# Kernel optimization log

Measured on AMD Instinct MI355X. Metric: run time of the kernel, lower is better.

The kernel has to match this reference:

```python
import jax, jax.numpy as jnp
import numpy as np

N_NODES = 50000
IN_DIM = 256
OUT_DIM = 128
NUM_HEADS = 2
N_EDGES = 800000


def setup_inputs() -> dict:
    key = jax.random.key(0)
    k1, k2, k3, k4, k5 = jax.random.split(key, 5)
    x = jax.random.normal(k1, (N_NODES, IN_DIM), dtype=jnp.float32)
    edge_index = jax.random.randint(k2, (2, N_EDGES), 0, N_NODES, dtype=jnp.int64)
    # Linear(in_dim, out_dim*num_heads): store weight as [in_dim, out_dim*num_heads]
    fan = IN_DIM + OUT_DIM * NUM_HEADS
    W_w = jax.random.uniform(k3, (IN_DIM, OUT_DIM * NUM_HEADS), dtype=jnp.float32,
                             minval=-np.sqrt(6.0 / fan), maxval=np.sqrt(6.0 / fan))
    W_b = jnp.zeros((OUT_DIM * NUM_HEADS,), dtype=jnp.float32)
    # attention vector a: [2*out_dim], xavier uniform over (1, 2*out_dim)
    fa = 1 + 2 * OUT_DIM
    a = jax.random.uniform(k4, (2 * OUT_DIM,), dtype=jnp.float32,
                           minval=-np.sqrt(6.0 / fa), maxval=np.sqrt(6.0 / fa))
    return {"x": x, "edge_index": edge_index, "W_w": W_w, "W_b": W_b, "a": a}


def _gat_forward(x, edge_index, W_w, W_b, a):
    N = x.shape[0]
    H, D = NUM_HEADS, OUT_DIM
    Wh = (x @ W_w + W_b).reshape(N, H, D)  # [N, H, D]
    src, dst = edge_index[0], edge_index[1]
    a_src, a_dst = a[:D], a[D:]
    # per-node partial scores, then gather -> avoids [E, 2D] concat
    s = jnp.einsum('nhd,d->nh', Wh, a_src)  # [N, H]
    t = jnp.einsum('nhd,d->nh', Wh, a_dst)  # [N, H]
    e = jax.nn.leaky_relu(s[src] + t[dst], negative_slope=0.2)  # [E, H]
    # segment softmax over edges grouped by src node
    m = jax.ops.segment_max(e, src, num_segments=N)  # [N, H], -inf for empty
    ex = jnp.exp(e - m[src])
    denom = jax.ops.segment_sum(ex, src, num_segments=N)  # [N, H]
    alpha = ex / denom[src]  # [E, H]
    # weighted aggregation of destination features into source nodes
    agg = jax.ops.segment_sum(alpha[:, :, None] * Wh[dst], src, num_segments=N)  # [N, H, D]
    deg = jax.ops.segment_sum(jnp.ones_like(src, dtype=Wh.dtype), src, num_segments=N)  # [N]
    h_prime = jnp.where(deg[:, None, None] > 0, agg, Wh)
    return h_prime.reshape(N, H * D)


def reference(x, edge_index, W_w, W_b, a):
    return _gat_forward(x, edge_index, W_w, W_b, a)
```

## Files before the change

### kernel.cpp

```cpp
#include <hip/hip_runtime.h>
#include <hip/hip_bf16.h>
#include <math.h>

#define N_NODES 50000
#define IN_DIM 256
#define OUT_DIM 128
#define NUM_HEADS 2
#define N_EDGES 800000
#define F (OUT_DIM*NUM_HEADS)
#define SCAN_B 1024
#define N_SB ((N_NODES + SCAN_B - 1) / SCAN_B)
#define LDSP 264
#define CAP 128
#define N_COPIES 8
#define NBLK ((N_NODES + 63) / 64)
#define GSZ (NBLK * 256)

typedef __bf16 bf16;
typedef __bf16 bf16x8 __attribute__((ext_vector_type(8)));
typedef float  f32x4  __attribute__((ext_vector_type(4)));
typedef unsigned short u16x8 __attribute__((ext_vector_type(8)));

__global__ void k_transpose(const float* __restrict__ W, bf16* __restrict__ Wt,
                            int* __restrict__ deg8) {
    int k = blockIdx.x;
    int n = threadIdx.x;
    Wt[(size_t)n*IN_DIM + k] = (bf16)W[(size_t)k*F + n];
    int id = blockIdx.x * F + threadIdx.x;
    for (int i = id; i < N_COPIES * N_NODES; i += IN_DIM * F)
        deg8[i] = 0;
}

__global__ __launch_bounds__(256) void k_gemm(const float* __restrict__ X,
                                              const bf16* __restrict__ Wt,
                                              const float* __restrict__ Wb,
                                              const float* __restrict__ Av,
                                              const int* __restrict__ src,
                                              int* __restrict__ deg8,
                                              unsigned char* __restrict__ rank,
                                              int* __restrict__ xcdtab,
                                              bf16* __restrict__ Wh,
                                              float* __restrict__ s_arr,
                                              float* __restrict__ t_arr) {
    __shared__ bf16 As[64 * LDSP];
    __shared__ float sS[2][64], sT[2][64];
    int t = threadIdx.x;
    int wave = t >> 6, lane = t & 63;
    int quad = lane >> 4, l16 = lane & 15;
    int row0 = blockIdx.x * 64;
    int col0 = wave * 64;
    int h = wave >> 1;

    {
        unsigned xcc;
        asm volatile("s_getreg_b32 %0, hwreg(HW_REG_XCC_ID, 0, 4)" : "=s"(xcc));
        xcc &= (N_COPIES - 1);
        if (t == 0) xcdtab[blockIdx.x] = (int)xcc;
        int* mydeg = deg8 + (size_t)xcc * N_NODES;
        int gid = blockIdx.x * 256 + t;
        for (int e = gid; e < N_EDGES; e += GSZ) {
            int s = src[e];
            int r = __hip_atomic_fetch_add(&mydeg[s], 1, __ATOMIC_RELAXED,
                                           __HIP_MEMORY_SCOPE_WORKGROUP);
            rank[e] = (unsigned char)r;
        }
    }

    {
        int rr = t >> 5;
        int cc = (t & 31) * 8;
        #pragma unroll
        for (int i = 0; i < 8; ++i) {
            int r = row0 + 8*i + rr;
            r = (r < N_NODES) ? r : (N_NODES - 1);
            const float* p = X + (size_t)r * IN_DIM + cc;
            f32x4 lo = *(const f32x4*)p;
            f32x4 hi = *(const f32x4*)(p + 4);
            bf16x8 pk;
            #pragma unroll
            for (int q = 0; q < 4; ++q) {
                pk[q]   = (bf16)lo[q];
                pk[q+4] = (bf16)hi[q];
            }
            *(bf16x8*)(As + (8*i + rr) * LDSP + cc) = pk;
        }
    }
    if (t < 128) { sS[t >> 6][t & 63] = 0.f; sT[t >> 6][t & 63] = 0.f; }
    __syncthreads();

    f32x4 acc[4][4] = {};
    #pragma unroll
    for (int ks = 0; ks < 8; ++ks) {
        int kb = ks * 32;
        bf16x8 bfrag[4];
        #pragma unroll
        for (int ni = 0; ni < 4; ++ni)
            bfrag[ni] = *(const bf16x8*)(Wt + (size_t)(col0 + ni*16 + l16)*IN_DIM
                                            + kb + quad*8);
        bf16x8 afrag[4];
        #pragma unroll
        for (int mi = 0; mi < 4; ++mi)
            afrag[mi] = *(const bf16x8*)(As + (mi*16 + l16)*LDSP + kb + quad*8);

        #pragma unroll
        for (int mi = 0; mi < 4; ++mi)
            #pragma unroll
            for (int ni = 0; ni < 4; ++ni)
                acc[mi][ni] = __builtin_amdgcn_mfma_f32_16x16x32_bf16(
                                  afrag[mi], bfrag[ni], acc[mi][ni], 0, 0, 0);
    }

    float bias_l[4], as_l[4], at_l[4];
    #pragma unroll
    for (int ni = 0; ni < 4; ++ni) {
        int c = col0 + ni*16 + l16;
        int d = c & (OUT_DIM - 1);
        bias_l[ni] = Wb[c];
        as_l[ni]   = Av[d];
        at_l[ni]   = Av[OUT_DIM + d];
    }

    #pragma unroll
    for (int mi = 0; mi < 4; ++mi) {
        #pragma unroll
        for (int reg = 0; reg < 4; ++reg) {
            int rl = mi*16 + quad*4 + reg;
            float ps = 0.f, pt = 0.f;
            #pragma unroll
            for (int ni = 0; ni < 4; ++ni) {
                float val = acc[mi][ni][reg] + bias_l[ni];
                ps += val * as_l[ni];
                pt += val * at_l[ni];
            }
            #pragma unroll
            for (int m = 8; m >= 1; m >>= 1) {
                ps += __shfl_xor(ps, m);
                pt += __shfl_xor(pt, m);
            }
            if ((lane & 15) == 0) {
                atomicAdd(&sS[h][rl], ps);
                atomicAdd(&sT[h][rl], pt);
            }
        }
    }

    __syncthreads();
    #pragma unroll
    for (int mi = 0; mi < 4; ++mi)
        #pragma unroll
        for (int ni = 0; ni < 4; ++ni) {
            int cc = col0 + ni*16 + l16;
            #pragma unroll
            for (int reg = 0; reg < 4; ++reg) {
                int rl = mi*16 + quad*4 + reg;
                As[rl*LDSP + cc] = (bf16)(acc[mi][ni][reg] + bias_l[ni]);
            }
        }
    __syncthreads();

    #pragma unroll
    for (int i = 0; i < 8; ++i) {
        int idx = i * 2048 + t * 8;
        int row = idx >> 8;
        int cc  = idx & 255;
        bf16x8 v = *(const bf16x8*)(As + row*LDSP + cc);
        int grow = row0 + row;
        if (grow < N_NODES)
            *(bf16x8*)(Wh + (size_t)grow*F + cc) = v;
    }

    if (t < 128) {
        int hh = t >> 6, rl = t & 63;
        int n = row0 + rl;
        if (n < N_NODES) {
            s_arr[n*2 + hh] = sS[hh][rl];
            t_arr[n*2 + hh] = sT[hh][rl];
        }
    }
}

__global__ __launch_bounds__(SCAN_B) void k_scan_local(const int* __restrict__ deg8,
                                                       int* __restrict__ excl,
                                                       int* __restrict__ bsum,
                                                       unsigned short* __restrict__ prefix8) {
    __shared__ int lds[SCAN_B];
    int t = threadIdx.x;
    int i = blockIdx.x * SCAN_B + t;
    int v = 0;
    if (i < N_NODES) {
        u16x8 pf;
        int run = 0;
        #pragma unroll
        for (int c = 0; c < N_COPIES; ++c) {
            pf[c] = (unsigned short)run;
            run += deg8[(size_t)c * N_NODES + i];
        }
        v = run;
        *(u16x8*)(prefix8 + (size_t)i * 8) = pf;
    }
    lds[t] = v;
    __syncthreads();
    for (int off = 1; off < SCAN_B; off <<= 1) {
        int u = (t >= off) ? lds[t - off] : 0;
        __syncthreads();
        lds[t] += u;
        __syncthreads();
    }
    if (i < N_NODES) excl[i] = lds[t] - v;
    if (t == SCAN_B - 1) bsum[blockIdx.x] = lds[t];
}

__global__ __launch_bounds__(256) void k_scan_final(const int* __restrict__ excl,
                                                    const int* __restrict__ bsum,
                                                    int* __restrict__ row_start) {
    __shared__ int sboff[64];
    int t = threadIdx.x;
    if (t < 64) {
        int orig = (t < N_SB) ? bsum[t] : 0;
        int v = orig;
        #pragma unroll
        for (int off = 1; off < 64; off <<= 1) {
            int u = __shfl_up(v, off);
            if (t >= off) v += u;
        }
        sboff[t] = v - orig;
        if (t == 63 && blockIdx.x == 0) row_start[N_NODES] = v;
    }
    __syncthreads();
    int i = blockIdx.x * 256 + t;
    if (i < N_NODES)
        row_start[i] = excl[i] + sboff[i >> 10];
}

__global__ __launch_bounds__(256) void k_scatter(const int* __restrict__ src,
                                                 const int* __restrict__ dst,
                                                 const unsigned char* __restrict__ rank,
                                                 const unsigned short* __restrict__ prefix8,
                                                 const int* __restrict__ row_start,
                                                 const int* __restrict__ xcdtab,
                                                 int* __restrict__ sorted_dst) {
    int e = blockIdx.x * 256 + threadIdx.x;
    if (e < N_EDGES) {
        int c = xcdtab[(e % GSZ) >> 8];
        int s = src[e];
        int pos = row_start[s] + (int)prefix8[(size_t)s * 8 + c] + (int)rank[e];
        sorted_dst[pos] = dst[e];
    }
}

__global__ __launch_bounds__(256) void k_agg(const bf16* __restrict__ Wh,
                                             const float* __restrict__ s_arr,
                                             const float* __restrict__ t_arr,
                                             const int* __restrict__ row_start,
                                             const int* __restrict__ sdst,
                                             float* __restrict__ out) {
    __shared__ float sp0[4][CAP];
    __shared__ float sp1[4][CAP];
    __shared__ int   sd[4][CAP];
    int wave = threadIdx.x >> 6, lane = threadIdx.x & 63;
    int n = blockIdx.x * 4 + wave;
    int sub = lane >> 5, cl = lane & 31;
    int c = cl * 8, h = cl >> 4;
    int beg = row_start[n], end = row_start[n + 1];
    if (beg == end) {
        if (sub == 0) {
            bf16x8 wh = *(const bf16x8*)(Wh + (size_t)n*F + c);
            f32x4 o0, o1;
            #pragma unroll
            for (int i = 0; i < 4; ++i) { o0[i] = (float)wh[i]; o1[i] = (float)wh[4+i]; }
            *(f32x4*)(out + (size_t)n*F + c)     = o0;
            *(f32x4*)(out + (size_t)n*F + c + 4) = o1;
        }
        return;
    }
    float2 sv = ((const float2*)s_arr)[n];
    float sum0 = 0.f, sum1 = 0.f;
    float a[8] = {0,0,0,0,0,0,0,0};
    float bacc[8] = {0,0,0,0,0,0,0,0};
    const float* sph = h ? sp1[wave] : sp0[wave];

    for (int c0 = beg; c0 < end; c0 += CAP) {
        int cnt = min(CAP, end - c0);
        for (int j = lane; j < cnt; j += 64) {
            int d = sdst[c0 + j];
            float2 tv = ((const float2*)t_arr)[d];
            float e0 = sv.x + tv.x; e0 = (e0 >= 0.f) ? e0 : 0.2f * e0;
            float e1 = sv.y + tv.y; e1 = (e1 >= 0.f) ? e1 : 0.2f * e1;
            float p0 = __expf(e0), p1 = __expf(e1);
            sp0[wave][j] = p0;
            sp1[wave][j] = p1;
            sd[wave][j]  = d;
            sum0 += p0;
            sum1 += p1;
        }
        int j = 0;
        for (; j + 8 <= cnt; j += 8) {
            int j0 = j + sub, j1 = j + 2 + sub, j2 = j + 4 + sub, j3 = j + 6 + sub;
            int d0 = sd[wave][j0], d1 = sd[wave][j1];
            int d2 = sd[wave][j2], d3 = sd[wave][j3];
            float p0 = sph[j0], p1 = sph[j1], p2 = sph[j2], p3 = sph[j3];
            bf16x8 w0 = *(const bf16x8*)(Wh + (size_t)d0*F + c);
            bf16x8 w1 = *(const bf16x8*)(Wh + (size_t)d1*F + c);
            bf16x8 w2 = *(const bf16x8*)(Wh + (size_t)d2*F + c);
            bf16x8 w3 = *(const bf16x8*)(Wh + (size_t)d3*F + c);
            #pragma unroll
            for (int i = 0; i < 8; ++i) {
                a[i]    += p0 * (float)w0[i];
                bacc[i] += p1 * (float)w1[i];
                a[i]    += p2 * (float)w2[i];
                bacc[i] += p3 * (float)w3[i];
            }
        }
        for (; j < cnt; j += 2) {
            int jj = j + sub;
            int jc = (jj < cnt) ? jj : 0;
            float p = (jj < cnt) ? sph[jc] : 0.f;
            int d = sd[wave][jc];
            bf16x8 w = *(const bf16x8*)(Wh + (size_t)d*F + c);
            #pragma unroll
            for (int i = 0; i < 8; ++i) a[i] += p * (float)w[i];
        }
    }
    #pragma unroll
    for (int m = 32; m >= 1; m >>= 1) {
        sum0 += __shfl_xor(sum0, m);
        sum1 += __shfl_xor(sum1, m);
    }
    float inv = 1.f / (h ? sum1 : sum0);
    #pragma unroll
    for (int i = 0; i < 8; ++i) {
        a[i] += bacc[i];
        a[i] += __shfl_xor(a[i], 32);
    }
    if (sub == 0) {
        f32x4 o0, o1;
        #pragma unroll
        for (int i = 0; i < 4; ++i) { o0[i] = a[i] * inv; o1[i] = a[4+i] * inv; }
        *(f32x4*)(out + (size_t)n*F + c)     = o0;
        *(f32x4*)(out + (size_t)n*F + c + 4) = o1;
    }
}

extern "C" void kernel_launch(void* const* d_in, const int* in_sizes, int n_in,
                              void* d_out, int out_size, void* d_ws, size_t ws_size,
                              hipStream_t stream) {
    const float* x  = (const float*)d_in[0];
    const int*   ei = (const int*)d_in[1];
    const float* Ww = (const float*)d_in[2];
    const float* Wb = (const float*)d_in[3];
    const float* a  = (const float*)d_in[4];
    float* out = (float*)d_out;
    const int* src = ei;
    const int* dst = ei + N_EDGES;

    char* ws = (char*)d_ws;
    bf16*  Wh        = (bf16*)ws;   ws += (size_t)N_NODES * F * 2;
    bf16*  Wt        = (bf16*)ws;   ws += (size_t)IN_DIM * F * 2;
    float* s_arr     = (float*)ws;  ws += (size_t)N_NODES * 2 * 4;
    float* t_arr     = (float*)ws;  ws += (size_t)N_NODES * 2 * 4;
    int*   excl      = (int*)ws;    ws += (size_t)N_NODES * 4;
    int*   bsum      = (int*)ws;    ws += 64 * 4;
    int*   row_start = (int*)ws;    ws += (size_t)(N_NODES + 1) * 4 + 12;
    unsigned short* prefix8 = (unsigned short*)ws; ws += (size_t)N_NODES * 8 * 2;
    unsigned char*  rank    = (unsigned char*)ws;  ws += (size_t)N_EDGES + 16;
    int*   xcdtab    = (int*)ws;    ws += (size_t)NBLK * 4 + 8;
    int*   sdst      = (int*)ws;    ws += (size_t)N_EDGES * 4;

    int* deg8 = sdst;

    k_transpose<<<IN_DIM, F, 0, stream>>>(Ww, Wt, deg8);
    k_gemm<<<NBLK, 256, 0, stream>>>(x, Wt, Wb, a, src, deg8, rank, xcdtab,
                                     Wh, s_arr, t_arr);
    k_scan_local<<<N_SB, SCAN_B, 0, stream>>>(deg8, excl, bsum, prefix8);
    k_scan_final<<<(N_NODES + 255) / 256, 256, 0, stream>>>(excl, bsum, row_start);
    k_scatter<<<(N_EDGES + 255) / 256, 256, 0, stream>>>(src, dst, rank, prefix8,
                                                         row_start, xcdtab, sdst);
    k_agg<<<N_NODES / 4, 256, 0, stream>>>(Wh, s_arr, t_arr, row_start, sdst, out);
}
```

Before: 244.9 us.

## Split edge histogram out of GEMM into a dedicated per-edge kernel

Moves the per-XCC source-degree atomic histogram and rank computation from the GEMM kernel's prologue into a separate kernel with one thread per edge. The scatter kernel now indexes the XCC table by block index directly and drops the modulo and bounds check. This is meant to remove the atomic work and grid-stride loop from the GEMM's critical path, at the cost of an extra kernel launch and losing the overlap between histogramming and GEMM loads.

```diff
diff --git a/kernel.cpp b/kernel.cpp
--- a/kernel.cpp
+++ b/kernel.cpp
@@ -13,8 +13,7 @@
 #define LDSP 264
 #define CAP 128
 #define N_COPIES 8
-#define NBLK ((N_NODES + 63) / 64)
-#define GSZ (NBLK * 256)
+#define NBLK_H (N_EDGES / 256)
 
 typedef __bf16 bf16;
 typedef __bf16 bf16x8 __attribute__((ext_vector_type(8)));
@@ -31,14 +30,25 @@
         deg8[i] = 0;
 }
 
+__global__ __launch_bounds__(256) void k_hist(const int* __restrict__ src,
+                                              int* __restrict__ deg8,
+                                              unsigned char* __restrict__ rank,
+                                              int* __restrict__ xcdtab) {
+    unsigned xcc;
+    asm volatile("s_getreg_b32 %0, hwreg(HW_REG_XCC_ID, 0, 4)" : "=s"(xcc));
+    xcc &= (N_COPIES - 1);
+    if (threadIdx.x == 0) xcdtab[blockIdx.x] = (int)xcc;
+    int e = blockIdx.x * 256 + threadIdx.x;
+    int s = src[e];
+    int r = __hip_atomic_fetch_add(&deg8[(size_t)xcc * N_NODES + s], 1,
+                                   __ATOMIC_RELAXED, __HIP_MEMORY_SCOPE_WORKGROUP);
+    rank[e] = (unsigned char)r;
+}
+
 __global__ __launch_bounds__(256) void k_gemm(const float* __restrict__ X,
                                               const bf16* __restrict__ Wt,
                                               const float* __restrict__ Wb,
                                               const float* __restrict__ Av,
-                                              const int* __restrict__ src,
-                                              int* __restrict__ deg8,
-                                              unsigned char* __restrict__ rank,
-                                              int* __restrict__ xcdtab,
                                               bf16* __restrict__ Wh,
                                               float* __restrict__ s_arr,
                                               float* __restrict__ t_arr) {
@@ -52,21 +62,6 @@
     int h = wave >> 1;
 
     {
-        unsigned xcc;
-        asm volatile("s_getreg_b32 %0, hwreg(HW_REG_XCC_ID, 0, 4)" : "=s"(xcc));
-        xcc &= (N_COPIES - 1);
-        if (t == 0) xcdtab[blockIdx.x] = (int)xcc;
-        int* mydeg = deg8 + (size_t)xcc * N_NODES;
-        int gid = blockIdx.x * 256 + t;
-        for (int e = gid; e < N_EDGES; e += GSZ) {
-            int s = src[e];
-            int r = __hip_atomic_fetch_add(&mydeg[s], 1, __ATOMIC_RELAXED,
-                                           __HIP_MEMORY_SCOPE_WORKGROUP);
-            rank[e] = (unsigned char)r;
-        }
-    }
-
-    {
         int rr = t >> 5;
         int cc = (t & 31) * 8;
         #pragma unroll
@@ -240,12 +235,10 @@
                                                  const int* __restrict__ xcdtab,
                                                  int* __restrict__ sorted_dst) {
     int e = blockIdx.x * 256 + threadIdx.x;
-    if (e < N_EDGES) {
-        int c = xcdtab[(e % GSZ) >> 8];
-        int s = src[e];
-        int pos = row_start[s] + (int)prefix8[(size_t)s * 8 + c] + (int)rank[e];
-        sorted_dst[pos] = dst[e];
-    }
+    int c = xcdtab[blockIdx.x];
+    int s = src[e];
+    int pos = row_start[s] + (int)prefix8[(size_t)s * 8 + c] + (int)rank[e];
+    sorted_dst[pos] = dst[e];
 }
 
 __global__ __launch_bounds__(256) void k_agg(const bf16* __restrict__ Wh,
@@ -363,17 +356,17 @@
     int*   row_start = (int*)ws;    ws += (size_t)(N_NODES + 1) * 4 + 12;
     unsigned short* prefix8 = (unsigned short*)ws; ws += (size_t)N_NODES * 8 * 2;
     unsigned char*  rank    = (unsigned char*)ws;  ws += (size_t)N_EDGES + 16;
-    int*   xcdtab    = (int*)ws;    ws += (size_t)NBLK * 4 + 8;
+    int*   xcdtab    = (int*)ws;    ws += (size_t)NBLK_H * 4 + 12;
     int*   sdst      = (int*)ws;    ws += (size_t)N_EDGES * 4;
 
     int* deg8 = sdst;
 
     k_transpose<<<IN_DIM, F, 0, stream>>>(Ww, Wt, deg8);
-    k_gemm<<<NBLK, 256, 0, stream>>>(x, Wt, Wb, a, src, deg8, rank, xcdtab,
-                                     Wh, s_arr, t_arr);
+    k_hist<<<NBLK_H, 256, 0, stream>>>(src, deg8, rank, xcdtab);
+    k_gemm<<<(N_NODES + 63) / 64, 256, 0, stream>>>(x, Wt, Wb, a, Wh, s_arr, t_arr);
     k_scan_local<<<N_SB, SCAN_B, 0, stream>>>(deg8, excl, bsum, prefix8);
     k_scan_final<<<(N_NODES + 255) / 256, 256, 0, stream>>>(excl, bsum, row_start);
-    k_scatter<<<(N_EDGES + 255) / 256, 256, 0, stream>>>(src, dst, rank, prefix8,
-                                                         row_start, xcdtab, sdst);
+    k_scatter<<<NBLK_H, 256, 0, stream>>>(src, dst, rank, prefix8,
+                                          row_start, xcdtab, sdst);
     k_agg<<<N_NODES / 4, 256, 0, stream>>>(Wh, s_arr, t_arr, row_start, sdst, out);
 }
```

Result: slower. 253.7 us (+3.6%).
